# Performance work log

Measured on AMD Instinct MI355X. Metric: run time of the kernel, lower is better.

Reference implementation:

```python
import jax, jax.numpy as jnp
import numpy as np

N_EMB = 2048
EMB_DIM = 512
EPS_IN = 1e-5  # instance-norm epsilon (torch default used in instance_norm)


def setup_inputs() -> dict:
    key = jax.random.key(0)
    kx, ke = jax.random.split(key)
    x = jax.random.normal(kx, (32, 1024, EMB_DIM), dtype=jnp.float32)
    # codebook init: uniform(-1/M, 1/M), then row-normalized (as in __init__)
    init_bound = 1.0 / N_EMB
    emb = jax.random.uniform(ke, (N_EMB, EMB_DIM), dtype=jnp.float32,
                             minval=-init_bound, maxval=init_bound)
    emb = emb / (jnp.linalg.norm(emb, axis=1, keepdims=True) + 1e-4)
    return {"x": x, "embedding": emb}


def _instance_norm(x, axis, eps=EPS_IN):
    mu = jnp.mean(x, axis=axis, keepdims=True)
    # torch.std default is unbiased (ddof=1)
    std = jnp.std(x, axis=axis, keepdims=True, ddof=1)
    return (x - mu) / (std + eps)


def reference(x, embedding):
    N, T, D = x.shape
    M = embedding.shape[0]
    z = _instance_norm(x, axis=1)  # normalize over time dim

    # normalized codebook only used for distance computation
    emb_n = embedding / (jnp.linalg.norm(embedding, axis=1, keepdims=True) + 1e-4)

    z_flat = jax.lax.stop_gradient(z).reshape(-1, D)  # (N*T, D)
    # ||e||^2 + ||z||^2 - 2 z.e  (addmm with alpha=-2, beta=1)
    distances = (jnp.sum(emb_n ** 2, axis=1)[None, :]
                 + jnp.sum(z_flat ** 2, axis=1, keepdims=True)
                 - 2.0 * (z_flat @ emb_n.T))  # (N*T, M)
    indices = jnp.argmin(distances.astype(jnp.float32), axis=-1)  # (N*T,)

    # lookup uses the UN-normalized embedding buffer (as in original)
    quantized = embedding[indices].reshape(N, T, D)

    commitment_loss = jnp.mean((z - jax.lax.stop_gradient(quantized)) ** 2)

    quantized_ste = z + jax.lax.stop_gradient(quantized - z)
    quantized_out = (quantized_ste + quantized) / 2.0

    # avg_probs = mean of one-hot encodings == normalized histogram
    counts = jnp.zeros((M,), dtype=jnp.float32).at[indices].add(1.0)
    avg_probs = counts / z_flat.shape[0]
    perplexity = jnp.exp(-jnp.sum(avg_probs * jnp.log(avg_probs + 1e-10)))

    return quantized_out, commitment_loss, perplexity
```

## Files before the change

### kernel.cpp

```cpp
#include <hip/hip_runtime.h>

#define T_DIM 1024
#define D_DIM 512
#define M_CODES 2048
#define NT 32768
#define TOTAL 16777216

typedef float f32x16 __attribute__((ext_vector_type(16)));
typedef unsigned int u32;
typedef unsigned long long u64;

#define WS_MU    0
#define WS_S     65536
#define WS_CE    131072
#define WS_DEN   139264
#define WS_CEU   147456
#define WS_CZ    155648
#define WS_KEYS  286720
#define WS_EB    548864
#define WS_HIST  (548864 + 1048576)
#define WS_LPART (WS_HIST + 8192)

__device__ __forceinline__ void gload16(const void* g, void* l) {
    __builtin_amdgcn_global_load_lds(
        (const __attribute__((address_space(1))) u32*)g,
        (__attribute__((address_space(3))) u32*)l, 16, 0, 0);
}

__device__ __forceinline__ float block_reduce_sum_256(float v) {
    #pragma unroll
    for (int s = 32; s; s >>= 1) v += __shfl_xor(v, s, 64);
    __shared__ float ls[4];
    int w = threadIdx.x >> 6;
    if ((threadIdx.x & 63) == 0) ls[w] = v;
    __syncthreads();
    float r = (ls[0] + ls[1]) + (ls[2] + ls[3]);
    __syncthreads();
    return r;
}

__device__ __forceinline__ u32 pk_fp8x4(float a, float b, float c, float d) {
    u32 w = __builtin_amdgcn_cvt_pk_fp8_f32(a, b, 0, false);
    w = __builtin_amdgcn_cvt_pk_fp8_f32(c, d, w, true);
    return w;
}

__device__ __forceinline__ u32 mono(float f) {
    u32 u = __float_as_uint(f);
    return u ^ (0x80000000u | (u32)((int)u >> 31));
}
__device__ __forceinline__ float unmono(u32 m) {
    u32 u = (m & 0x80000000u) ? (m ^ 0x80000000u) : ~m;
    return __uint_as_float(u);
}

__device__ __forceinline__ int pk_dest(int d, int row) {
    return (d & ~31) | ((((d >> 3) & 3) ^ ((row >> 2) & 3)) << 3) | (d & 7);
}

__global__ void prep_kernel(const float* __restrict__ x, const float* __restrict__ emb,
                            float* __restrict__ mu_o, float* __restrict__ s_o,
                            unsigned char* __restrict__ eb, float* __restrict__ cen,
                            float* __restrict__ den_o, float* __restrict__ ceu) {
    int bx = blockIdx.x;
    if (bx < M_CODES) {
        int j = bx;
        int d = threadIdx.x * 2;
        float2 e = *(const float2*)&emb[(size_t)j * D_DIM + d];
        float sq = e.x * e.x + e.y * e.y;
        float norm2 = block_reduce_sum_256(sq);
        float den = sqrtf(norm2) + 1e-4f;
        float en0 = e.x / den, en1 = e.y / den;
        u32 w = __builtin_amdgcn_cvt_pk_fp8_f32(en0, en1, 0, false);
        *(unsigned short*)&eb[(size_t)j * D_DIM + pk_dest(d, j)] =
            (unsigned short)(w & 0xFFFF);
        float cep = en0 * en0 + en1 * en1;
        float cesum = block_reduce_sum_256(cep);
        if (threadIdx.x == 0) { cen[j] = cesum; den_o[j] = den; ceu[j] = norm2; }
    } else {
        int idx = bx - M_CODES;
        int n = idx >> 3;
        int lane = threadIdx.x & 63;
        int d = (idx & 7) * 64 + lane;
        int tg = threadIdx.x >> 6;
        const float* xp = x + (size_t)n * (T_DIM * D_DIM) + d;
        float sum = 0.f, sq = 0.f;
        int t0 = tg * 256;
        for (int it = 0; it < 256; ++it) {
            float v = xp[(size_t)(t0 + it) * D_DIM];
            sum += v; sq += v * v;
        }
        __shared__ float ssum[4][64], ssq[4][64];
        ssum[tg][lane] = sum;
        ssq[tg][lane] = sq;
        __syncthreads();
        if (threadIdx.x < 64) {
            int l = threadIdx.x;
            float s1 = (ssum[0][l] + ssum[1][l]) + (ssum[2][l] + ssum[3][l]);
            float q1 = (ssq[0][l] + ssq[1][l]) + (ssq[2][l] + ssq[3][l]);
            float mu = s1 * (1.0f / 1024.0f);
            float var = (q1 - 1024.0f * mu * mu) * (1.0f / 1023.0f);
            var = fmaxf(var, 0.0f);
            float sd = sqrtf(var) + 1e-5f;
            int nd = n * D_DIM + (idx & 7) * 64 + l;
            mu_o[nd] = mu; s_o[nd] = sd;
        }
    }
}

__global__ void pack_kernel(const float* __restrict__ x, const float* __restrict__ mu,
                            const float* __restrict__ s, unsigned char* __restrict__ zq,
                            float* __restrict__ cz) {
    int i = blockIdx.x * 4 + (threadIdx.x >> 6);
    int lane = threadIdx.x & 63;
    int n = i >> 10;
    const float* xp = x + (size_t)i * D_DIM;
    const float* mp = mu + n * D_DIM;
    const float* sp = s + n * D_DIM;
    float acc = 0.f;
    #pragma unroll
    for (int c = 0; c < 2; ++c) {
        int d = c * 256 + lane * 4;
        float4 xv = *(const float4*)&xp[d];
        float4 mv = *(const float4*)&mp[d];
        float4 sv = *(const float4*)&sp[d];
        float z0 = (xv.x - mv.x) / sv.x;
        float z1 = (xv.y - mv.y) / sv.y;
        float z2 = (xv.z - mv.z) / sv.z;
        float z3 = (xv.w - mv.w) / sv.w;
        *(u32*)&zq[(size_t)i * D_DIM + pk_dest(d, i)] = pk_fp8x4(z0, z1, z2, z3);
        acc += z0 * z0 + z1 * z1 + z2 * z2 + z3 * z3;
    }
    #pragma unroll
    for (int sft = 32; sft; sft >>= 1) acc += __shfl_xor(acc, sft, 64);
    if (lane == 0) cz[i] = acc;
}

__global__ __launch_bounds__(512, 2) void gemm_argmin(
    const unsigned char* __restrict__ zq, const unsigned char* __restrict__ eb,
    const float* __restrict__ ce, u64* __restrict__ keys) {
    __shared__ long smem[4][2048];
    int tid = threadIdx.x;
    int bid = blockIdx.x;
    int swz = (bid & 7) * 128 + (bid >> 3);
    int n0 = (swz & 7) * 256;
    int m0 = (swz >> 3) * 256;

    f32x16 acc[2][4];
    #pragma unroll
    for (int a = 0; a < 2; ++a)
        #pragma unroll
        for (int b = 0; b < 4; ++b) acc[a][b] = (f32x16)0.0f;

    int w = tid >> 6, l = tid & 63;
    int wm = (w >> 1) * 64;
    int wn = (w & 1) * 128;
    int lr = l & 31;
    int lk = l >> 5;

    int rS = 32 * w + (l >> 1);
    int hS = (l & 1) * 16;
    size_t srcA = (size_t)(m0 + rS) * D_DIM + hS;
    size_t srcB = (size_t)(n0 + rS) * D_DIM + hS;

    #define STAGE(buf, t) do {                                                    \
        gload16(zq + srcA + (t) * 32, &smem[buf][w * 128]);                       \
        gload16(eb + srcB + (t) * 32, &smem[buf][1024 + w * 128]);                \
    } while (0)

    STAGE(0, 0);
    STAGE(1, 1);
    STAGE(2, 2);
    asm volatile("s_waitcnt vmcnt(4)" ::: "memory");
    __builtin_amdgcn_s_barrier();
    __builtin_amdgcn_sched_barrier(0);

    for (int t = 0; t < 16; ++t) {
        int cur = t & 3;
        if (t <= 12) STAGE((t + 3) & 3, t + 3);
        long av[2][2], bv[4][2];
        #pragma unroll
        for (int mi = 0; mi < 2; ++mi) {
            int r = wm + mi * 32 + lr;
            int xr = (r >> 2) & 3;
            #pragma unroll
            for (int h = 0; h < 2; ++h)
                av[mi][h] = smem[cur][r * 4 + (((h << 1) + lk) ^ xr)];
        }
        #pragma unroll
        for (int ni = 0; ni < 4; ++ni) {
            int r = wn + ni * 32 + lr;
            int xr = (r >> 2) & 3;
            #pragma unroll
            for (int h = 0; h < 2; ++h)
                bv[ni][h] = smem[cur][1024 + r * 4 + (((h << 1) + lk) ^ xr)];
        }
        __builtin_amdgcn_s_setprio(1);
        #pragma unroll
        for (int mi = 0; mi < 2; ++mi)
            #pragma unroll
            for (int ni = 0; ni < 4; ++ni) {
                acc[mi][ni] = __builtin_amdgcn_mfma_f32_32x32x16_fp8_fp8(
                    av[mi][0], bv[ni][0], acc[mi][ni], 0, 0, 0);
                acc[mi][ni] = __builtin_amdgcn_mfma_f32_32x32x16_fp8_fp8(
                    av[mi][1], bv[ni][1], acc[mi][ni], 0, 0, 0);
            }
        __builtin_amdgcn_s_setprio(0);
        if (t < 15) {
            if (t <= 12)      asm volatile("s_waitcnt vmcnt(4)" ::: "memory");
            else if (t == 13) asm volatile("s_waitcnt vmcnt(2)" ::: "memory");
            else              asm volatile("s_waitcnt vmcnt(0)" ::: "memory");
            __builtin_amdgcn_s_barrier();
            __builtin_amdgcn_sched_barrier(0);
        }
    }
    #undef STAGE

    #pragma unroll
    for (int mi = 0; mi < 2; ++mi) {
        #pragma unroll
        for (int reg = 0; reg < 16; ++reg) {
            int qrow = m0 + wm + mi * 32 + (reg & 3) + 8 * (reg >> 2) + 4 * lk;
            u64 best = ~0ULL;
            #pragma unroll
            for (int ni = 0; ni < 4; ++ni) {
                int j = n0 + wn + ni * 32 + lr;
                float dist = ce[j] - 2.0f * acc[mi][ni][reg];
                u64 key = ((u64)mono(dist) << 32) | (unsigned)j;
                if (key < best) best = key;
            }
            #pragma unroll
            for (int sft = 1; sft < 32; sft <<= 1) {
                u64 o = __shfl_xor(best, sft, 64);
                if (o < best) best = o;
            }
            if (lr == 0) atomicMin(keys + qrow, best);
        }
    }
}

__global__ void finish_kernel(const float* __restrict__ emb,
                              const u64* __restrict__ keys,
                              const float* __restrict__ cz,
                              const float* __restrict__ cen,
                              const float* __restrict__ den,
                              const float* __restrict__ ceu,
                              float* __restrict__ out,
                              float* __restrict__ loss_part,
                              unsigned* __restrict__ hist) {
    int i = blockIdx.x * 4 + (threadIdx.x >> 6);
    int lane = threadIdx.x & 63;
    u64 kk = keys[i];
    unsigned idx = (u32)kk;
    #pragma unroll
    for (int c = 0; c < 2; ++c) {
        int d = c * 256 + lane * 4;
        float4 ev = *(const float4*)&emb[(size_t)idx * D_DIM + d];
        *(float4*)&out[(size_t)i * D_DIM + d] = ev;
    }
    __shared__ float ls[4];
    if (lane == 0) {
        float dist = unmono((u32)(kk >> 32));
        ls[threadIdx.x >> 6] = cz[i] + (dist - cen[idx]) * den[idx] + ceu[idx];
        atomicAdd(&hist[idx], 1u);
    }
    __syncthreads();
    if (threadIdx.x == 0)
        loss_part[blockIdx.x] = (ls[0] + ls[1]) + (ls[2] + ls[3]);
}

__global__ void final_kernel(const unsigned* __restrict__ hist,
                             const float* __restrict__ loss_part, float* __restrict__ out) {
    float h = 0.f;
    for (int b = threadIdx.x; b < M_CODES; b += 256) {
        float p = (float)hist[b] * (1.0f / 32768.0f);
        h += p * logf(p + 1e-10f);
    }
    h = block_reduce_sum_256(h);
    float lsum = 0.f;
    for (int b = threadIdx.x; b < NT / 4; b += 256) lsum += loss_part[b];
    lsum = block_reduce_sum_256(lsum);
    if (threadIdx.x == 0) {
        out[TOTAL] = lsum * (1.0f / 16777216.0f);
        out[TOTAL + 1] = expf(-h);
    }
}

extern "C" void kernel_launch(void* const* d_in, const int* in_sizes, int n_in,
                              void* d_out, int out_size, void* d_ws, size_t ws_size,
                              hipStream_t stream) {
    (void)in_sizes; (void)n_in; (void)out_size; (void)ws_size;
    const float* x = (const float*)d_in[0];
    const float* emb = (const float*)d_in[1];
    float* out = (float*)d_out;
    char* ws = (char*)d_ws;
    float* mu   = (float*)(ws + WS_MU);
    float* s    = (float*)(ws + WS_S);
    float* cen  = (float*)(ws + WS_CE);
    float* den  = (float*)(ws + WS_DEN);
    float* ceu  = (float*)(ws + WS_CEU);
    float* cz   = (float*)(ws + WS_CZ);
    u64* keys = (u64*)(ws + WS_KEYS);
    unsigned char* eb = (unsigned char*)(ws + WS_EB);
    unsigned* hist = (unsigned*)(ws + WS_HIST);
    float* loss_part = (float*)(ws + WS_LPART);
    unsigned char* zq = (unsigned char*)d_out;

    (void)hipMemsetAsync(ws + WS_KEYS, 0xFF, 262144, stream);
    (void)hipMemsetAsync(ws + WS_HIST, 0x00, 8192, stream);

    prep_kernel<<<M_CODES + 256, 256, 0, stream>>>(x, emb, mu, s, eb, cen, den, ceu);
    pack_kernel<<<NT / 4, 256, 0, stream>>>(x, mu, s, zq, cz);
    gemm_argmin<<<1024, 512, 0, stream>>>(zq, eb, cen, keys);
    finish_kernel<<<NT / 4, 256, 0, stream>>>(emb, keys, cz, cen, den, ceu,
                                              out, loss_part, hist);
    final_kernel<<<1, 256, 0, stream>>>(hist, loss_part, out);
}
```

Before: 155.4 us.

## Switch fp8 GEMM to scaled 32x32x64 MFMA with K=64 tiles

Replaces the pair of 32x32x16 fp8 MFMAs per k-step with the MI355 scaled f8f6f4 32x32x64 MFMA using unit scales. The K tile grows from 32 to 64, so the pipeline has 8 iterations with triple buffering instead of 16 with quad buffering. The fp8 pre-swizzle of zq/eb is changed to 16-byte chunks so the wider LDS reads avoid bank conflicts. This aims to cut MFMA issue count and barrier overhead per K, at the cost of larger LDS stages and fewer stages in flight.

```diff
diff --git a/kernel.cpp b/kernel.cpp
--- a/kernel.cpp
+++ b/kernel.cpp
@@ -7,6 +7,8 @@
 #define TOTAL 16777216
 
 typedef float f32x16 __attribute__((ext_vector_type(16)));
+typedef int i32x4 __attribute__((ext_vector_type(4)));
+typedef int i32x8 __attribute__((ext_vector_type(8)));
 typedef unsigned int u32;
 typedef unsigned long long u64;
 
@@ -54,8 +56,8 @@
     return __uint_as_float(u);
 }
 
-__device__ __forceinline__ int pk_dest(int d, int row) {
-    return (d & ~31) | ((((d >> 3) & 3) ^ ((row >> 2) & 3)) << 3) | (d & 7);
+__device__ __forceinline__ int pk16(int d, int row) {
+    return (d & ~63) | ((((d >> 4) & 3) ^ (row & 3)) << 4) | (d & 15);
 }
 
 __global__ void prep_kernel(const float* __restrict__ x, const float* __restrict__ emb,
@@ -72,7 +74,7 @@
         float den = sqrtf(norm2) + 1e-4f;
         float en0 = e.x / den, en1 = e.y / den;
         u32 w = __builtin_amdgcn_cvt_pk_fp8_f32(en0, en1, 0, false);
-        *(unsigned short*)&eb[(size_t)j * D_DIM + pk_dest(d, j)] =
+        *(unsigned short*)&eb[(size_t)j * D_DIM + pk16(d, j)] =
             (unsigned short)(w & 0xFFFF);
         float cep = en0 * en0 + en1 * en1;
         float cesum = block_reduce_sum_256(cep);
@@ -128,7 +130,7 @@
         float z1 = (xv.y - mv.y) / sv.y;
         float z2 = (xv.z - mv.z) / sv.z;
         float z3 = (xv.w - mv.w) / sv.w;
-        *(u32*)&zq[(size_t)i * D_DIM + pk_dest(d, i)] = pk_fp8x4(z0, z1, z2, z3);
+        *(u32*)&zq[(size_t)i * D_DIM + pk16(d, i)] = pk_fp8x4(z0, z1, z2, z3);
         acc += z0 * z0 + z1 * z1 + z2 * z2 + z3 * z3;
     }
     #pragma unroll
@@ -139,7 +141,7 @@
 __global__ __launch_bounds__(512, 2) void gemm_argmin(
     const unsigned char* __restrict__ zq, const unsigned char* __restrict__ eb,
     const float* __restrict__ ce, u64* __restrict__ keys) {
-    __shared__ long smem[4][2048];
+    __shared__ char smem[3][32768];
     int tid = threadIdx.x;
     int bid = blockIdx.x;
     int swz = (bid & 7) * 128 + (bid >> 3);
@@ -157,62 +159,64 @@
     int wn = (w & 1) * 128;
     int lr = l & 31;
     int lk = l >> 5;
-
-    int rS = 32 * w + (l >> 1);
-    int hS = (l & 1) * 16;
-    size_t srcA = (size_t)(m0 + rS) * D_DIM + hS;
-    size_t srcB = (size_t)(n0 + rS) * D_DIM + hS;
+    const int sc = 0x7F7F7F7F;
 
     #define STAGE(buf, t) do {                                                    \
-        gload16(zq + srcA + (t) * 32, &smem[buf][w * 128]);                       \
-        gload16(eb + srcB + (t) * 32, &smem[buf][1024 + w * 128]);                \
+        _Pragma("unroll")                                                         \
+        for (int q = 0; q < 2; ++q) {                                             \
+            int rr = 32 * w + 16 * q + (l >> 2);                                  \
+            size_t off = (size_t)(t) * 64 + (l & 3) * 16;                         \
+            gload16(zq + (size_t)(m0 + rr) * D_DIM + off,                         \
+                    &smem[buf][(32 * w + 16 * q) * 64]);                          \
+            gload16(eb + (size_t)(n0 + rr) * D_DIM + off,                         \
+                    &smem[buf][16384 + (32 * w + 16 * q) * 64]);                  \
+        }                                                                         \
     } while (0)
 
     STAGE(0, 0);
     STAGE(1, 1);
-    STAGE(2, 2);
     asm volatile("s_waitcnt vmcnt(4)" ::: "memory");
     __builtin_amdgcn_s_barrier();
     __builtin_amdgcn_sched_barrier(0);
 
-    for (int t = 0; t < 16; ++t) {
-        int cur = t & 3;
-        if (t <= 12) STAGE((t + 3) & 3, t + 3);
-        long av[2][2], bv[4][2];
+    int rd = 0, wr = 2;
+    for (int t = 0; t < 8; ++t) {
+        if (t <= 5) STAGE(wr, t + 2);
+        i32x8 av[2], bv[4];
         #pragma unroll
         for (int mi = 0; mi < 2; ++mi) {
             int r = wm + mi * 32 + lr;
-            int xr = (r >> 2) & 3;
-            #pragma unroll
-            for (int h = 0; h < 2; ++h)
-                av[mi][h] = smem[cur][r * 4 + (((h << 1) + lk) ^ xr)];
+            int x3 = r & 3;
+            const char* Ab = &smem[rd][r * 64];
+            i32x4 p0 = *(const i32x4*)(Ab + (((lk << 1)    ) ^ x3) * 16);
+            i32x4 p1 = *(const i32x4*)(Ab + (((lk << 1) + 1) ^ x3) * 16);
+            av[mi] = __builtin_shufflevector(p0, p1, 0, 1, 2, 3, 4, 5, 6, 7);
         }
         #pragma unroll
         for (int ni = 0; ni < 4; ++ni) {
             int r = wn + ni * 32 + lr;
-            int xr = (r >> 2) & 3;
-            #pragma unroll
-            for (int h = 0; h < 2; ++h)
-                bv[ni][h] = smem[cur][1024 + r * 4 + (((h << 1) + lk) ^ xr)];
+            int x3 = r & 3;
+            const char* Bb = &smem[rd][16384 + r * 64];
+            i32x4 p0 = *(const i32x4*)(Bb + (((lk << 1)    ) ^ x3) * 16);
+            i32x4 p1 = *(const i32x4*)(Bb + (((lk << 1) + 1) ^ x3) * 16);
+            bv[ni] = __builtin_shufflevector(p0, p1, 0, 1, 2, 3, 4, 5, 6, 7);
         }
         __builtin_amdgcn_s_setprio(1);
         #pragma unroll
         for (int mi = 0; mi < 2; ++mi)
             #pragma unroll
-            for (int ni = 0; ni < 4; ++ni) {
-                acc[mi][ni] = __builtin_amdgcn_mfma_f32_32x32x16_fp8_fp8(
-                    av[mi][0], bv[ni][0], acc[mi][ni], 0, 0, 0);
-                acc[mi][ni] = __builtin_amdgcn_mfma_f32_32x32x16_fp8_fp8(
-                    av[mi][1], bv[ni][1], acc[mi][ni], 0, 0, 0);
-            }
+            for (int ni = 0; ni < 4; ++ni)
+                acc[mi][ni] = __builtin_amdgcn_mfma_scale_f32_32x32x64_f8f6f4(
+                    av[mi], bv[ni], acc[mi][ni], 0, 0, 0, sc, 0, sc);
         __builtin_amdgcn_s_setprio(0);
-        if (t < 15) {
-            if (t <= 12)      asm volatile("s_waitcnt vmcnt(4)" ::: "memory");
-            else if (t == 13) asm volatile("s_waitcnt vmcnt(2)" ::: "memory");
-            else              asm volatile("s_waitcnt vmcnt(0)" ::: "memory");
+        if (t < 7) {
+            if (t <= 5) asm volatile("s_waitcnt vmcnt(4)" ::: "memory");
+            else        asm volatile("s_waitcnt vmcnt(0)" ::: "memory");
             __builtin_amdgcn_s_barrier();
             __builtin_amdgcn_sched_barrier(0);
         }
+        if (++rd == 3) rd = 0;
+        if (++wr == 3) wr = 0;
     }
     #undef STAGE
 
```

Result: slower. 232.9 us (+49.9%).
